# Performance work log

Hardware: AMD Instinct MI355X
Metric: run time of the kernel (lower is better)

## Reference

```python
import jax, jax.numpy as jnp
import numpy as np

B, N, E, P, NH = 8, 1024, 768, 768, 12
HD = P // NH


def setup_inputs() -> dict:
    key = jax.random.key(0)
    ks = jax.random.split(key, 9)
    s = lambda k, sh: jax.random.normal(k, sh, dtype=jnp.float32) * 0.02
    return {
        "x": jax.random.normal(ks[0], (B, N, E), dtype=jnp.float32),
        "wq": s(ks[1], (E, P)), "bq": jnp.zeros((P,), jnp.float32),
        "wk": s(ks[2], (E, P)), "bk": jnp.zeros((P,), jnp.float32),
        "wv": s(ks[3], (E, P)), "bv": jnp.zeros((P,), jnp.float32),
        "wo": s(ks[4], (P, E)), "bo": jnp.zeros((E,), jnp.float32),
        "H": 32, "W": 32,
    }


def reference(x, wq, bq, wk, bk, wv, bv, wo, bo, H, W):
    b, n, _ = x.shape
    # QKV projections: [B,N,P] -> [B,NH,N,HD]
    def split_heads(t):
        return t.reshape(b, n, NH, HD).transpose(0, 2, 1, 3)
    q = split_heads(x @ wq + bq)
    k = split_heads(x @ wk + bk)
    v = split_heads(x @ wv + bv)
    # NOTE: original module applies NO 1/sqrt(head_dim) scaling.
    logits = jnp.einsum("bhqd,bhkd->bhqk", q, k)  # [B,NH,N,N]
    attn = jax.nn.softmax(logits, axis=-1)
    ctx = jnp.einsum("bhqk,bhkd->bhqd", attn, v)  # [B,NH,N,HD]
    ctx = ctx.transpose(0, 2, 1, 3).reshape(b, n, P)
    return ctx @ wo + bo
```

## Files before the change

### kernel.cpp

```cpp
#include <hip/hip_runtime.h>
#include <hip/hip_bf16.h>
#include <math.h>

#define B_   8
#define N_   1024
#define E_   768
#define P_   768
#define NH_  12
#define HD_  64
#define L2E  1.44269504088896340736f

typedef __attribute__((ext_vector_type(8))) short short8;
typedef __attribute__((ext_vector_type(4))) float f32x4;

__device__ inline void async16(void* lds, const void* g) {
    __builtin_amdgcn_global_load_lds(
        (const __attribute__((address_space(1))) void*)g,
        (__attribute__((address_space(3))) void*)lds, 16, 0, 0);
}

__device__ inline unsigned pkbf(float a, float b) {
    union { float f; unsigned u; } ua, ub;
    ua.f = a; ub.f = b;
    return __builtin_amdgcn_perm(ub.u, ua.u, 0x07060302u);
}

__global__ __launch_bounds__(256) void cvt_x(const float* __restrict__ x,
                                             __hip_bfloat16* __restrict__ xb, int n4) {
    int i = blockIdx.x * blockDim.x + threadIdx.x;
    const int stride = gridDim.x * blockDim.x;
    for (; i < n4; i += stride) {
        float4 f = ((const float4*)x)[i];
        union { __hip_bfloat16 h[4]; uint2 u; } pk;
        pk.h[0] = __float2bfloat16(f.x);
        pk.h[1] = __float2bfloat16(f.y);
        pk.h[2] = __float2bfloat16(f.z);
        pk.h[3] = __float2bfloat16(f.w);
        ((uint2*)xb)[i] = pk.u;
    }
}

__global__ __launch_bounds__(256) void cvt_tw(
    const float* __restrict__ W0, const float* __restrict__ W1,
    const float* __restrict__ W2, const float* __restrict__ W3,
    __hip_bfloat16* __restrict__ T0, __hip_bfloat16* __restrict__ T1,
    __hip_bfloat16* __restrict__ T2, __hip_bfloat16* __restrict__ T3) {
    const int z = blockIdx.z;
    const float* W = (z == 0) ? W0 : (z == 1) ? W1 : (z == 2) ? W2 : W3;
    __hip_bfloat16* T = (z == 0) ? T0 : (z == 1) ? T1 : (z == 2) ? T2 : T3;
    __shared__ float t[32][33];
    const int tx = threadIdx.x & 31, ty = threadIdx.x >> 5;
    const int n0 = blockIdx.x * 32, k0 = blockIdx.y * 32;
#pragma unroll
    for (int rr = 0; rr < 4; ++rr)
        t[ty + rr * 8][tx] = W[(k0 + ty + rr * 8) * 768 + n0 + tx];
    __syncthreads();
#pragma unroll
    for (int rr = 0; rr < 4; ++rr)
        T[(long)(n0 + ty + rr * 8) * 768 + k0 + tx] = __float2bfloat16(t[tx][ty + rr * 8]);
}

__global__ __launch_bounds__(256) void gemm_bf16(
    const __hip_bfloat16* __restrict__ A0, const __hip_bfloat16* __restrict__ A1,
    const __hip_bfloat16* __restrict__ Bp,
    const float* __restrict__ bias0, const float* __restrict__ bias1,
    void* __restrict__ C0, void* __restrict__ C1, int mode) {
    __shared__ __hip_bfloat16 As[2 * 128 * 32];
    __shared__ __hip_bfloat16 Bs[2 * 128 * 32];

    int z = 0, xb6 = blockIdx.x;
    if (mode == 2) { z = blockIdx.x / 6; xb6 = blockIdx.x % 6; }
    const __hip_bfloat16* Arows = z ? A1 : A0;
    const float* bias = z ? bias1 : bias0;
    void* Cout = z ? C1 : C0;

    const int tid = threadIdx.x;
    const int lane = tid & 63;
    const int w = tid >> 6;
    const int l15 = lane & 15;
    const int quad = lane >> 4;
    const int mh = (w >> 1) * 64;
    const int nh = (w & 1) * 64;
    const int rb = (mode >= 2) ? xb6 * 128 : blockIdx.y * 128;
    const int cb = (mode >= 2) ? blockIdx.y * 128 : xb6 * 128;

    f32x4 acc[4][4];
#pragma unroll
    for (int i = 0; i < 4; ++i)
#pragma unroll
        for (int j = 0; j < 4; ++j) acc[i][j] = (f32x4){0.f, 0.f, 0.f, 0.f};

    const int c0 = tid, c1 = tid + 256;
    const __hip_bfloat16* gA0 = Arows + (long)(rb + (c0 >> 2)) * 768 + (c0 & 3) * 8;
    const __hip_bfloat16* gA1 = Arows + (long)(rb + (c1 >> 2)) * 768 + (c1 & 3) * 8;
    const __hip_bfloat16* gB0 = Bp + (long)(cb + (c0 >> 2)) * 768 + (c0 & 3) * 8;
    const __hip_bfloat16* gB1 = Bp + (long)(cb + (c1 >> 2)) * 768 + (c1 & 3) * 8;
    const int o0 = c0 * 16, o1 = c1 * 16;

    async16((char*)As + o0, gA0);
    async16((char*)As + o1, gA1);
    async16((char*)Bs + o0, gB0);
    async16((char*)Bs + o1, gB1);

    for (int it = 0; it < 24; ++it) {
        const int bo = (it & 1) * 8192;
        const int no = 8192 - bo;
        __syncthreads();
        if (it + 1 < 24) {
            const int k1 = (it + 1) * 32;
            async16((char*)As + no + o0, gA0 + k1);
            async16((char*)As + no + o1, gA1 + k1);
            async16((char*)Bs + no + o0, gB0 + k1);
            async16((char*)Bs + no + o1, gB1 + k1);
        }

        short8 a[4], b[4];
#pragma unroll
        for (int i = 0; i < 4; ++i)
            a[i] = *(const short8*)((char*)As + bo + ((mh + i * 16 + l15) * 32 + quad * 8) * 2);
#pragma unroll
        for (int j = 0; j < 4; ++j)
            b[j] = *(const short8*)((char*)Bs + bo + ((nh + j * 16 + l15) * 32 + quad * 8) * 2);
#pragma unroll
        for (int i = 0; i < 4; ++i)
#pragma unroll
            for (int j = 0; j < 4; ++j)
                acc[i][j] = __builtin_amdgcn_mfma_f32_16x16x32_bf16(a[i], b[j], acc[i][j], 0, 0, 0);
    }

    if (mode == 2) {
        __hip_bfloat16* O = (__hip_bfloat16*)Cout;
#pragma unroll
        for (int j = 0; j < 4; ++j) {
            const int n = cb + nh + j * 16 + l15;
            const int bb = n >> 10, nn = n & 1023;
#pragma unroll
            for (int i = 0; i < 4; ++i) {
                const int p0 = rb + mh + i * 16 + quad * 4;
                const int h = p0 >> 6, d0 = p0 & 63;
                const float4 bv = *(const float4*)(bias + p0);
                union { __hip_bfloat16 h4[4]; unsigned long long u; } pk;
                pk.h4[0] = __float2bfloat16(acc[i][j][0] + bv.x);
                pk.h4[1] = __float2bfloat16(acc[i][j][1] + bv.y);
                pk.h4[2] = __float2bfloat16(acc[i][j][2] + bv.z);
                pk.h4[3] = __float2bfloat16(acc[i][j][3] + bv.w);
                *(unsigned long long*)(O + (((long)(bb * NH_ + h)) * N_ + nn) * HD_ + d0) = pk.u;
            }
        }
    } else if (mode == 1) {
        __hip_bfloat16* O = (__hip_bfloat16*)Cout;
#pragma unroll
        for (int j = 0; j < 4; ++j) {
            const int p = cb + nh + j * 16 + l15;
            const int h = p >> 6, d = p & 63;
            const float bv = bias[p];
#pragma unroll
            for (int i = 0; i < 4; ++i) {
                const int n0 = rb + mh + i * 16 + quad * 4;
                const int bb = n0 >> 10, nn = n0 & 1023;
                union { __hip_bfloat16 h4[4]; unsigned long long u; } pk;
#pragma unroll
                for (int r = 0; r < 4; ++r)
                    pk.h4[r] = __float2bfloat16(acc[i][j][r] + bv);
                *(unsigned long long*)(O + (((long)(bb * NH_ + h)) * HD_ + d) * N_ + nn) = pk.u;
            }
        }
    } else {
        float* O = (float*)Cout;
#pragma unroll
        for (int j = 0; j < 4; ++j) {
            const int n = cb + nh + j * 16 + l15;
#pragma unroll
            for (int i = 0; i < 4; ++i) {
                const int e0 = rb + mh + i * 16 + quad * 4;
                const float4 bv = *(const float4*)(bias + e0);
                float4 vo;
                vo.x = acc[i][j][0] + bv.x;
                vo.y = acc[i][j][1] + bv.y;
                vo.z = acc[i][j][2] + bv.z;
                vo.w = acc[i][j][3] + bv.w;
                *(float4*)(O + (long)n * 768 + e0) = vo;
            }
        }
    }
}

__global__ __launch_bounds__(256, 3) void attn_mfma(
    const __hip_bfloat16* __restrict__ Q, const __hip_bfloat16* __restrict__ K,
    const __hip_bfloat16* __restrict__ Vt, __hip_bfloat16* __restrict__ ctx) {
    __shared__ __hip_bfloat16 Ks[2 * 64 * 64];
    __shared__ __hip_bfloat16 Vs[2 * 64 * 64];

    const int tid = threadIdx.x;
    const int lane = tid & 63, w = tid >> 6;
    const int l15 = lane & 15, quad = lane >> 4;
    const int y3 = l15 & 7;

    const int bx = blockIdx.x;
    const int rr_ = bx & 7, t_ = bx >> 3;
    const int qb = t_ & 7, hi_ = t_ >> 3;
    const int H = hi_ * 8 + rr_;
    const int bz = H / 12, hy = H - bz * 12;
    const long headOff = (long)H * (N_ * HD_);
    const int qBase = qb * 128;

    short8 qf[2][2];
#pragma unroll
    for (int i = 0; i < 2; ++i)
#pragma unroll
        for (int ks = 0; ks < 2; ++ks)
            qf[i][ks] = *(const short8*)(Q + headOff +
                (long)(qBase + w * 32 + i * 16 + l15) * HD_ + ks * 32 + quad * 8);

    f32x4 o[4][2];
#pragma unroll
    for (int mt = 0; mt < 4; ++mt)
#pragma unroll
        for (int i = 0; i < 2; ++i) o[mt][i] = (f32x4){0.f, 0.f, 0.f, 0.f};
    f32x4 ol[2];
    ol[0] = (f32x4){0.f, 0.f, 0.f, 0.f};
    ol[1] = (f32x4){0.f, 0.f, 0.f, 0.f};
    const short8 onesv = (short8){0x3F80, 0x3F80, 0x3F80, 0x3F80,
                                  0x3F80, 0x3F80, 0x3F80, 0x3F80};

    const int p0 = tid, p1 = tid + 256;
    const int r0 = p0 >> 3, lc0 = (p0 & 7) ^ (r0 & 7);
    const int r1 = p1 >> 3, lc1 = (p1 & 7) ^ (r1 & 7);
    const __hip_bfloat16* gK0 = K + headOff + r0 * HD_ + lc0 * 8;
    const __hip_bfloat16* gK1 = K + headOff + r1 * HD_ + lc1 * 8;
    const __hip_bfloat16* gV0 = Vt + headOff + r0 * N_ + lc0 * 8;
    const __hip_bfloat16* gV1 = Vt + headOff + r1 * N_ + lc1 * 8;
    const int q0 = p0 * 16, q1 = p1 * 16;

    async16((char*)Ks + q0, gK0);
    async16((char*)Ks + q1, gK1);
    async16((char*)Vs + q0, gV0);
    async16((char*)Vs + q1, gV1);

    for (int it = 0; it < 16; ++it) {
        const int bo = (it & 1) * 8192;
        const int no = 8192 - bo;
        __syncthreads();
        if (it + 1 < 16) {
            const int j1 = (it + 1) * 64;
            async16((char*)Ks + no + q0, gK0 + (long)j1 * HD_);
            async16((char*)Ks + no + q1, gK1 + (long)j1 * HD_);
            async16((char*)Vs + no + q0, gV0 + j1);
            async16((char*)Vs + no + q1, gV1 + j1);
        }

        f32x4 sT[4][2];
#pragma unroll
        for (int n = 0; n < 4; ++n)
#pragma unroll
            for (int i = 0; i < 2; ++i) sT[n][i] = (f32x4){0.f, 0.f, 0.f, 0.f};
#pragma unroll
        for (int ks = 0; ks < 2; ++ks) {
            short8 kf[4];
#pragma unroll
            for (int n = 0; n < 4; ++n)
                kf[n] = *(const short8*)((char*)Ks + bo +
                    ((n * 16 + l15) * 64 + (((ks * 4 + quad) ^ y3) * 8)) * 2);
#pragma unroll
            for (int n = 0; n < 4; ++n)
#pragma unroll
                for (int i = 0; i < 2; ++i)
                    sT[n][i] = __builtin_amdgcn_mfma_f32_16x16x32_bf16(kf[n], qf[i][ks], sT[n][i], 0, 0, 0);
        }

        short8 pf[2][2];
#pragma unroll
        for (int i = 0; i < 2; ++i) {
            float pv[4][4];
#pragma unroll
            for (int n = 0; n < 4; ++n)
#pragma unroll
                for (int r = 0; r < 4; ++r)
                    pv[n][r] = __expf(sT[n][i][r] - 16.635532333438686f);
            union { unsigned u[4]; short8 v; } pk0, pk1;
            pk0.u[0] = pkbf(pv[0][0], pv[0][1]);
            pk0.u[1] = pkbf(pv[0][2], pv[0][3]);
            pk0.u[2] = pkbf(pv[1][0], pv[1][1]);
            pk0.u[3] = pkbf(pv[1][2], pv[1][3]);
            pk1.u[0] = pkbf(pv[2][0], pv[2][1]);
            pk1.u[1] = pkbf(pv[2][2], pv[2][3]);
            pk1.u[2] = pkbf(pv[3][0], pv[3][1]);
            pk1.u[3] = pkbf(pv[3][2], pv[3][3]);
            pf[i][0] = pk0.v;
            pf[i][1] = pk1.v;
        }

#pragma unroll
        for (int g = 0; g < 2; ++g) {
#pragma unroll
            for (int mt = 0; mt < 4; ++mt) {
                const int row = mt * 16 + l15;
                union { short s4[2][4]; short8 v; } vb;
#pragma unroll
                for (int h = 0; h < 2; ++h) {
                    const int chunk = g * 4 + h * 2 + (quad >> 1);
                    *(long*)vb.s4[h] = *(const long*)((char*)Vs + bo +
                        (row * 64 + ((chunk ^ y3) * 8 + (quad & 1) * 4)) * 2);
                }
#pragma unroll
                for (int i = 0; i < 2; ++i)
                    o[mt][i] = __builtin_amdgcn_mfma_f32_16x16x32_bf16(vb.v, pf[i][g], o[mt][i], 0, 0, 0);
            }
#pragma unroll
            for (int i = 0; i < 2; ++i)
                ol[i] = __builtin_amdgcn_mfma_f32_16x16x32_bf16(onesv, pf[i][g], ol[i], 0, 0, 0);
        }
    }

#pragma unroll
    for (int i = 0; i < 2; ++i) {
        const float inv = 1.0f / ol[i][0];
        const int q = qBase + w * 32 + i * 16 + l15;
        __hip_bfloat16* op = ctx + ((long)(bz * N_ + q)) * P_ + hy * HD_;
#pragma unroll
        for (int mt = 0; mt < 4; ++mt) {
            union { __hip_bfloat16 h[4]; unsigned long long u; } pk;
#pragma unroll
            for (int r = 0; r < 4; ++r)
                pk.h[r] = __float2bfloat16(o[mt][i][r] * inv);
            *(unsigned long long*)(op + mt * 16 + quad * 4) = pk.u;
        }
    }
}

extern "C" void kernel_launch(void* const* d_in, const int* in_sizes, int n_in,
                              void* d_out, int out_size, void* d_ws, size_t ws_size,
                              hipStream_t stream) {
    const float* x  = (const float*)d_in[0];
    const float* wq = (const float*)d_in[1];
    const float* bq = (const float*)d_in[2];
    const float* wk = (const float*)d_in[3];
    const float* bk = (const float*)d_in[4];
    const float* wv = (const float*)d_in[5];
    const float* bv = (const float*)d_in[6];
    const float* wo = (const float*)d_in[7];
    const float* bo = (const float*)d_in[8];
    float* out = (float*)d_out;

    char* p = (char*)d_ws;
    const long XB = (long)B_ * N_ * E_ * 2;
    const long WB = (long)E_ * P_ * 2;
    const long HB = (long)B_ * NH_ * N_ * HD_ * 2;
    __hip_bfloat16* xb  = (__hip_bfloat16*)p; p += XB;
    __hip_bfloat16* wqt = (__hip_bfloat16*)p; p += WB;
    __hip_bfloat16* wkt = (__hip_bfloat16*)p; p += WB;
    __hip_bfloat16* wvt = (__hip_bfloat16*)p; p += WB;
    __hip_bfloat16* wot = (__hip_bfloat16*)p; p += WB;
    __hip_bfloat16* qh  = (__hip_bfloat16*)p; p += HB;
    __hip_bfloat16* kh  = (__hip_bfloat16*)p; p += HB;
    __hip_bfloat16* vth = (__hip_bfloat16*)p; p += HB;
    __hip_bfloat16* ctxb = (__hip_bfloat16*)p; p += HB;

    cvt_x<<<2048, 256, 0, stream>>>(x, xb, (B_ * N_ * E_) / 4);
    cvt_tw<<<dim3(24, 24, 4), 256, 0, stream>>>(wq, wk, wv, wo, wqt, wkt, wvt, wot);

    gemm_bf16<<<dim3(12, (B_ * N_) / 128), 256, 0, stream>>>(
        wqt, wkt, xb, bq, bk, qh, kh, 2);

    gemm_bf16<<<dim3(6, (B_ * N_) / 128), 256, 0, stream>>>(
        xb, xb, wvt, bv, bv, vth, vth, 1);

    attn_mfma<<<dim3(768), 256, 0, stream>>>(qh, kh, vth, ctxb);

    gemm_bf16<<<dim3(6, (B_ * N_) / 128), 256, 0, stream>>>(
        wot, wot, ctxb, bo, bo, out, out, 3);
}
```

Before: 234.0 us.

## Fuse QKV GEMMs into one launch, swizzle LDS, narrow output GEMM tile

The Q/K and V projection GEMMs now run as a single 1152-block launch that picks its mode from the block index, removing one kernel launch and the tail between them. The LDS tiles use an XOR swizzle on the 16-byte column chunk to reduce bank conflicts on the MFMA operand reads. The output projection moves to a 128x64 tile, doubling the block count to 768 for better CU occupancy. The cost is more branching in the kernel prologue and less reuse per block in the output GEMM.

Result: faster. 228.8 us (-2.2%).

```diff
diff --git a/kernel.cpp b/kernel.cpp
--- a/kernel.cpp
+++ b/kernel.cpp
@@ -60,19 +60,44 @@
         T[(long)(n0 + ty + rr * 8) * 768 + k0 + tx] = __float2bfloat16(t[tx][ty + rr * 8]);
 }
 
-__global__ __launch_bounds__(256) void gemm_bf16(
+template <int NC>
+__global__ __launch_bounds__(256) void gemm_core(
     const __hip_bfloat16* __restrict__ A0, const __hip_bfloat16* __restrict__ A1,
-    const __hip_bfloat16* __restrict__ Bp,
-    const float* __restrict__ bias0, const float* __restrict__ bias1,
-    void* __restrict__ C0, void* __restrict__ C1, int mode) {
-    __shared__ __hip_bfloat16 As[2 * 128 * 32];
-    __shared__ __hip_bfloat16 Bs[2 * 128 * 32];
-
-    int z = 0, xb6 = blockIdx.x;
-    if (mode == 2) { z = blockIdx.x / 6; xb6 = blockIdx.x % 6; }
-    const __hip_bfloat16* Arows = z ? A1 : A0;
-    const float* bias = z ? bias1 : bias0;
-    void* Cout = z ? C1 : C0;
+    const __hip_bfloat16* __restrict__ A2,
+    const __hip_bfloat16* __restrict__ B01, const __hip_bfloat16* __restrict__ B2,
+    const float* __restrict__ b0, const float* __restrict__ b1,
+    const float* __restrict__ b2,
+    void* __restrict__ C0, void* __restrict__ C1, void* __restrict__ C2,
+    int fused) {
+    constexpr int ABUF = 8192;
+    constexpr int BBUF = NC * 64;
+    constexpr int JT = NC / 32;
+    __shared__ char As[2 * ABUF];
+    __shared__ char Bs[2 * BBUF];
+
+    const __hip_bfloat16* Arows;
+    const __hip_bfloat16* Brows;
+    const float* bias;
+    void* Cout;
+    int mode, rb, cb;
+    if (fused) {
+        const int lin = blockIdx.x;
+        if (lin < 768) {
+            mode = 2;
+            const int y = lin / 12, r = lin % 12, z = r / 6;
+            rb = (r % 6) * 128; cb = y * 128;
+            Arows = z ? A1 : A0; Brows = B01; bias = z ? b1 : b0; Cout = z ? C1 : C0;
+        } else {
+            mode = 1;
+            const int t = lin - 768;
+            rb = (t / 6) * 128; cb = (t % 6) * 128;
+            Arows = A2; Brows = B2; bias = b2; Cout = C2;
+        }
+    } else {
+        mode = 3;
+        rb = (blockIdx.x % 6) * 128; cb = (blockIdx.x / 6) * NC;
+        Arows = A0; Brows = B01; bias = b0; Cout = C0;
+    }
 
     const int tid = threadIdx.x;
     const int lane = tid & 63;
@@ -80,58 +105,61 @@
     const int l15 = lane & 15;
     const int quad = lane >> 4;
     const int mh = (w >> 1) * 64;
-    const int nh = (w & 1) * 64;
-    const int rb = (mode >= 2) ? xb6 * 128 : blockIdx.y * 128;
-    const int cb = (mode >= 2) ? blockIdx.y * 128 : xb6 * 128;
-
-    f32x4 acc[4][4];
+    const int nh = (w & 1) * (NC / 2);
+
+    f32x4 acc[4][JT];
 #pragma unroll
     for (int i = 0; i < 4; ++i)
 #pragma unroll
-        for (int j = 0; j < 4; ++j) acc[i][j] = (f32x4){0.f, 0.f, 0.f, 0.f};
-
-    const int c0 = tid, c1 = tid + 256;
-    const __hip_bfloat16* gA0 = Arows + (long)(rb + (c0 >> 2)) * 768 + (c0 & 3) * 8;
-    const __hip_bfloat16* gA1 = Arows + (long)(rb + (c1 >> 2)) * 768 + (c1 & 3) * 8;
-    const __hip_bfloat16* gB0 = Bp + (long)(cb + (c0 >> 2)) * 768 + (c0 & 3) * 8;
-    const __hip_bfloat16* gB1 = Bp + (long)(cb + (c1 >> 2)) * 768 + (c1 & 3) * 8;
-    const int o0 = c0 * 16, o1 = c1 * 16;
-
-    async16((char*)As + o0, gA0);
-    async16((char*)As + o1, gA1);
-    async16((char*)Bs + o0, gB0);
-    async16((char*)Bs + o1, gB1);
+        for (int j = 0; j < JT; ++j) acc[i][j] = (f32x4){0.f, 0.f, 0.f, 0.f};
+
+    const int c1 = tid + 256;
+    const int ar0 = tid >> 2, alc0 = (tid & 3) ^ ((ar0 >> 1) & 3);
+    const int ar1 = c1 >> 2,  alc1 = (c1 & 3) ^ ((ar1 >> 1) & 3);
+    const __hip_bfloat16* gA0 = Arows + (long)(rb + ar0) * 768 + alc0 * 8;
+    const __hip_bfloat16* gA1 = Arows + (long)(rb + ar1) * 768 + alc1 * 8;
+    const __hip_bfloat16* gB0 = B01 ? (Brows + (long)(cb + ar0) * 768 + alc0 * 8) : nullptr;
+    const __hip_bfloat16* gB1 = (NC == 128) ? (Brows + (long)(cb + ar1) * 768 + alc1 * 8) : nullptr;
+
+    async16(As + tid * 16, gA0);
+    async16(As + c1 * 16, gA1);
+    async16(Bs + tid * 16, gB0);
+    if (NC == 128) async16(Bs + c1 * 16, gB1);
 
     for (int it = 0; it < 24; ++it) {
-        const int bo = (it & 1) * 8192;
-        const int no = 8192 - bo;
+        const int boA = (it & 1) * ABUF, noA = ABUF - boA;
+        const int boB = (it & 1) * BBUF, noB = BBUF - boB;
         __syncthreads();
         if (it + 1 < 24) {
             const int k1 = (it + 1) * 32;
-            async16((char*)As + no + o0, gA0 + k1);
-            async16((char*)As + no + o1, gA1 + k1);
-            async16((char*)Bs + no + o0, gB0 + k1);
-            async16((char*)Bs + no + o1, gB1 + k1);
-        }
-
-        short8 a[4], b[4];
+            async16(As + noA + tid * 16, gA0 + k1);
+            async16(As + noA + c1 * 16, gA1 + k1);
+            async16(Bs + noB + tid * 16, gB0 + k1);
+            if (NC == 128) async16(Bs + noB + c1 * 16, gB1 + k1);
+        }
+
+        short8 a[4], b[JT];
+#pragma unroll
+        for (int i = 0; i < 4; ++i) {
+            const int row = mh + i * 16 + l15;
+            a[i] = *(const short8*)(As + boA + row * 64 + (quad ^ ((row >> 1) & 3)) * 16);
+        }
+#pragma unroll
+        for (int j = 0; j < JT; ++j) {
+            const int row = nh + j * 16 + l15;
+            b[j] = *(const short8*)(Bs + boB + row * 64 + (quad ^ ((row >> 1) & 3)) * 16);
+        }
 #pragma unroll
         for (int i = 0; i < 4; ++i)
-            a[i] = *(const short8*)((char*)As + bo + ((mh + i * 16 + l15) * 32 + quad * 8) * 2);
-#pragma unroll
-        for (int j = 0; j < 4; ++j)
-            b[j] = *(const short8*)((char*)Bs + bo + ((nh + j * 16 + l15) * 32 + quad * 8) * 2);
-#pragma unroll
-        for (int i = 0; i < 4; ++i)
-#pragma unroll
-            for (int j = 0; j < 4; ++j)
+#pragma unroll
+            for (int j = 0; j < JT; ++j)
                 acc[i][j] = __builtin_amdgcn_mfma_f32_16x16x32_bf16(a[i], b[j], acc[i][j], 0, 0, 0);
     }
 
     if (mode == 2) {
         __hip_bfloat16* O = (__hip_bfloat16*)Cout;
 #pragma unroll
-        for (int j = 0; j < 4; ++j) {
+        for (int j = 0; j < JT; ++j) {
             const int n = cb + nh + j * 16 + l15;
             const int bb = n >> 10, nn = n & 1023;
 #pragma unroll
@@ -150,7 +178,7 @@
     } else if (mode == 1) {
         __hip_bfloat16* O = (__hip_bfloat16*)Cout;
 #pragma unroll
-        for (int j = 0; j < 4; ++j) {
+        for (int j = 0; j < JT; ++j) {
             const int p = cb + nh + j * 16 + l15;
             const int h = p >> 6, d = p & 63;
             const float bv = bias[p];
@@ -168,7 +196,7 @@
     } else {
         float* O = (float*)Cout;
 #pragma unroll
-        for (int j = 0; j < 4; ++j) {
+        for (int j = 0; j < JT; ++j) {
             const int n = cb + nh + j * 16 + l15;
 #pragma unroll
             for (int i = 0; i < 4; ++i) {
@@ -359,14 +387,11 @@
     cvt_x<<<2048, 256, 0, stream>>>(x, xb, (B_ * N_ * E_) / 4);
     cvt_tw<<<dim3(24, 24, 4), 256, 0, stream>>>(wq, wk, wv, wo, wqt, wkt, wvt, wot);
 
-    gemm_bf16<<<dim3(12, (B_ * N_) / 128), 256, 0, stream>>>(
-        wqt, wkt, xb, bq, bk, qh, kh, 2);
-
-    gemm_bf16<<<dim3(6, (B_ * N_) / 128), 256, 0, stream>>>(
-        xb, xb, wvt, bv, bv, vth, vth, 1);
+    gemm_core<128><<<dim3(1152), 256, 0, stream>>>(
+        wqt, wkt, xb, xb, wvt, bq, bk, bv, qh, kh, vth, 1);
 
     attn_mfma<<<dim3(768), 256, 0, stream>>>(qh, kh, vth, ctxb);
 
-    gemm_bf16<<<dim3(6, (B_ * N_) / 128), 256, 0, stream>>>(
-        wot, wot, ctxb, bo, bo, out, out, 3);
-}
+    gemm_core<64><<<dim3(768), 256, 0, stream>>>(
+        wot, wot, wot, ctxb, ctxb, bo, bo, bo, out, out, out, 0);
+}
```
